# Performance work log

Hardware: AMD Instinct MI355X
Metric: run time of the kernel (lower is better)

## Reference

```python
import jax, jax.numpy as jnp
import numpy as np

B, S, H, A = 16, 2048, 1024, 1024


def setup_inputs() -> dict:
    key = jax.random.key(0)
    k1, k2, k3 = jax.random.split(key, 3)
    x = jax.random.normal(k1, (B, S, H), dtype=jnp.float32)
    # learned params (nn.Parameter tensors in the torch module)
    w_a = jax.random.normal(k2, (H, A), dtype=jnp.float32) * 0.02
    query = jax.random.normal(k3, (H, A), dtype=jnp.float32) * 0.02
    return {"x": x, "w_a": w_a, "query": query}


def reference(x, w_a, query):
    # semantic attention: values = x
    key = jnp.tanh(x @ w_a)          # [B, S, A]
    q = x @ query                    # [B, S, A]  (per-token semantic query)
    # temp[b, s, t] = q[b, s] . key[b, t]
    temp = jnp.einsum('bsa,bta->bst', q, key)  # [B, S, S]
    seq_len = x.shape[1]
    # softmax mask: strictly-upper triangle = -inf, lower+diag = 0 (causal)
    causal = jnp.triu(jnp.ones((seq_len, seq_len), dtype=bool), k=1)
    softmax_mask = jnp.where(causal, -jnp.inf, 0.0).astype(x.dtype)
    d = jax.nn.softmax(temp + softmax_mask, axis=-1)  # [B, S, S]
    a = d @ x                        # [B, S, H]
    return (a, d)
```

## Files before the change

### kernel.cpp

```cpp
#include <hip/hip_runtime.h>

typedef _Float16 f16x8 __attribute__((ext_vector_type(8)));
typedef float f32x4 __attribute__((ext_vector_type(4)));
typedef unsigned short u16;
typedef u16 u16x4 __attribute__((ext_vector_type(4)));
typedef u16 u16x8 __attribute__((ext_vector_type(8)));

#define NBATCH 16
#define NSEQ   2048
#define NHID   1024
#define MALL   (NBATCH * NSEQ)

__device__ __forceinline__ u16 f16_rne(float x) {
    _Float16 h = (_Float16)x;
    return __builtin_bit_cast(u16, h);
}
__device__ __forceinline__ float fast_tanh(float x) {
    float e = __expf(2.0f * x);
    return 1.0f - 2.0f / (e + 1.0f);
}

#define GLOAD16(g, l) __builtin_amdgcn_global_lds(0)
#undef GLOAD16
#define GLOAD16(g, l) __builtin_amdgcn_global_load_lds(                         \
    (const __attribute__((address_space(1))) unsigned int*)(g),                 \
    (__attribute__((address_space(3))) unsigned int*)(l), 16, 0, 0)


#define NOPS ((void)0)
#define VMW4 asm volatile("s_waitcnt vmcnt(4)" ::: "memory");
#define VMW0 asm volatile("s_waitcnt vmcnt(0)" ::: "memory");

#define MMPH(MH, NH)                                                           \
    MM(acc[MH][NH][0][0], 0, (NH)*2+0); MM(acc[MH][NH][0][1], 0, (NH)*2+1);    \
    MM(acc[MH][NH][1][0], 1, (NH)*2+0); MM(acc[MH][NH][1][1], 1, (NH)*2+1);    \
    MM(acc[MH][NH][2][0], 2, (NH)*2+0); MM(acc[MH][NH][2][1], 2, (NH)*2+1);    \
    MM(acc[MH][NH][3][0], 3, (NH)*2+0); MM(acc[MH][NH][3][1], 3, (NH)*2+1);    \
    MM(acc[MH][NH][0][0], 4, (NH)*2+4); MM(acc[MH][NH][0][1], 4, (NH)*2+5);    \
    MM(acc[MH][NH][1][0], 5, (NH)*2+4); MM(acc[MH][NH][1][1], 5, (NH)*2+5);    \
    MM(acc[MH][NH][2][0], 6, (NH)*2+4); MM(acc[MH][NH][2][1], 6, (NH)*2+5);    \
    MM(acc[MH][NH][3][0], 7, (NH)*2+4); MM(acc[MH][NH][3][1], 7, (NH)*2+5);

#define PH_SYNC                                                                \
    __builtin_amdgcn_s_barrier();                                              \
    asm volatile("s_waitcnt lgkmcnt(0)" ::: "memory");                         \
    __builtin_amdgcn_sched_barrier(0);

#define TILE8(C, S1, S2, S3, S4, W) {                                          \
                                                                \
    LDA(0,C,0,0); LDA(1,C,0,0); LDA(2,C,0,0); LDA(3,C,0,0);                    \
    LDA(4,C,0,1); LDA(5,C,0,1); LDA(6,C,0,1); LDA(7,C,0,1);                    \
    LDB(0,C,0,0); LDB(1,C,0,0); LDB(4,C,0,1); LDB(5,C,0,1);                    \
    S1;                                                                        \
    PH_SYNC                                                                    \
    __builtin_amdgcn_s_setprio(1); MMPH(0,0) __builtin_amdgcn_s_setprio(0);    \
    __builtin_amdgcn_s_barrier();                                              \
                                                                \
    LDB(2,C,1,0); LDB(3,C,1,0); LDB(6,C,1,1); LDB(7,C,1,1);                    \
    S2;                                                                        \
    PH_SYNC                                                                    \
    __builtin_amdgcn_s_setprio(1); MMPH(0,1) __builtin_amdgcn_s_setprio(0);    \
    __builtin_amdgcn_s_barrier();                                              \
                                                                \
    LDA(0,C,1,0); LDA(1,C,1,0); LDA(2,C,1,0); LDA(3,C,1,0);                    \
    LDA(4,C,1,1); LDA(5,C,1,1); LDA(6,C,1,1); LDA(7,C,1,1);                    \
    S3;                                                                        \
    PH_SYNC                                                                    \
    __builtin_amdgcn_s_setprio(1); MMPH(1,0) __builtin_amdgcn_s_setprio(0);    \
    __builtin_amdgcn_s_barrier();                                              \
                                                                \
    S4;                                                                        \
    PH_SYNC                                                                    \
    __builtin_amdgcn_s_setprio(1); MMPH(1,1) __builtin_amdgcn_s_setprio(0);    \
    W;                                                                         \
    __builtin_amdgcn_s_barrier();                                              \
}

__device__ __forceinline__ void gemm_core64(
    const u16* __restrict__ Ap, int Arow0,
    const u16* __restrict__ Bp, int Brow0,
    u16* lds, f32x4 (&acc)[2][2][4][2])
{
    int tid = threadIdx.x;
    int l = tid & 63, w = tid >> 6;
    int wr = w >> 2, wc = w & 3;
    int fr = l & 15, sg = l >> 4;

    f16x8 ah[8], bh[8];

    auto LDA = [&](int i, int C, int MH, int KH) {
        int rb = MH * 128 + wr * 64 + (i & 3) * 16 + fr;
        int sl = ((KH * 4 + sg) ^ (rb & 7)) * 8;
        ah[i] = *(const f16x8*)&lds[C * 32768 + rb * 64 + sl];
    };
    auto LDB = [&](int j, int C, int NH, int KH) {
        int rb = NH * 128 + wc * 32 + (j & 1) * 16 + fr;
        int sl = ((KH * 4 + sg) ^ (rb & 7)) * 8;
        bh[j] = *(const f16x8*)&lds[C * 32768 + 16384 + rb * 64 + sl];
    };
    auto MM = [&](f32x4& d, int i, int j) {
        d = __builtin_amdgcn_mfma_f32_16x16x32_f16(ah[i], bh[j], d, 0, 0, 0);
    };
    auto STA = [&](int C, int H, int T) {
        int rg = Arow0 + H * 128 + w * 8 + (l >> 3);
        const u16* s = Ap + (size_t)rg * 1024 + (size_t)T * 64
                       + ((l & 7) ^ (rg & 7)) * 8;
        u16* d = &lds[C * 32768 + (H * 128 + w * 8) * 64];
        GLOAD16(s, d);
        GLOAD16(s + (size_t)64 * 1024, d + 64 * 64);
    };
    auto STB = [&](int C, int H, int T) {
        int rg = Brow0 + H * 128 + w * 8 + (l >> 3);
        const u16* s = Bp + (size_t)rg * 1024 + (size_t)T * 64
                       + ((l & 7) ^ (rg & 7)) * 8;
        u16* d = &lds[C * 32768 + 16384 + (H * 128 + w * 8) * 64];
        GLOAD16(s, d);
        GLOAD16(s + (size_t)64 * 1024, d + 64 * 64);
    };

    STA(0, 0, 0); STA(0, 1, 0); STB(0, 0, 0); STB(0, 1, 0);
    STA(1, 0, 1); STB(1, 0, 1);
    VMW4
    __builtin_amdgcn_s_barrier();

    for (int u = 0; u < 13; u += 2) {
        TILE8(0, STA(1,1,u+1), STB(1,1,u+1), STA(0,0,u+2), STB(0,0,u+2), VMW4)
        TILE8(1, STA(0,1,u+2), STB(0,1,u+2), STA(1,0,u+3), STB(1,0,u+3), VMW4)
    }
    TILE8(0, STA(1,1,15), STB(1,1,15), NOPS, NOPS, VMW0)
    TILE8(1, NOPS, NOPS, NOPS, NOPS, NOPS)
}

__global__ __launch_bounds__(256) void wprep_kernel(
    const float* __restrict__ wa, const float* __restrict__ qu,
    u16* __restrict__ wT)
{
    int idx = blockIdx.x * 256 + threadIdx.x;
    int h = idx >> 10, n = idx & 1023;
    wT[(size_t)n * 1024 + h]          = f16_rne(wa[idx] * 64.0f);
    wT[(size_t)(1024 + n) * 1024 + h] = f16_rne(qu[idx] * 64.0f);
}

__global__ __launch_bounds__(256) void xprep_kernel(
    const float* __restrict__ x, u16* __restrict__ xT,
    u16* __restrict__ x_f16)
{
    __shared__ u16 tile[64][68];
    int b = blockIdx.z;
    int t0 = blockIdx.x * 64;
    int h0 = blockIdx.y * 64;
    const float* xb = x + ((size_t)b * NSEQ + t0) * NHID + h0;
    int tid = threadIdx.x;
    int tl = tid >> 4;
    int hl = (tid & 15) * 4;
    #pragma unroll
    for (int i = 0; i < 4; i++) {
        int r = i * 16 + tl;
        float4 v = *(const float4*)&xb[(size_t)r * NHID + hl];
        u16x4 hv;
        hv[0] = f16_rne(v.x); hv[1] = f16_rne(v.y);
        hv[2] = f16_rne(v.z); hv[3] = f16_rne(v.w);
        *(u16x4*)&tile[r][hl] = hv;
        *(u16x4*)&x_f16[((size_t)(b * NSEQ) + t0 + r) * NHID + h0 + hl] = hv;
    }
    __syncthreads();
    u16* xTb = xT + ((size_t)b * NHID + h0) * NSEQ + t0;
    int hl2 = tid >> 4;
    int tl2 = (tid & 15) * 4;
    #pragma unroll
    for (int i = 0; i < 4; i++) {
        int hh = i * 16 + hl2;
        u16x4 o;
        o[0] = tile[tl2 + 0][hh]; o[1] = tile[tl2 + 1][hh];
        o[2] = tile[tl2 + 2][hh]; o[3] = tile[tl2 + 3][hh];
        *(u16x4*)&xTb[(size_t)hh * NSEQ + tl2] = o;
    }
}

__global__ __launch_bounds__(512, 2) void k1_gemm(
    const u16* __restrict__ x_f16, const u16* __restrict__ wT,
    u16* __restrict__ k_f16, u16* __restrict__ q_f16)
{
    extern __shared__ u16 lds[];
    int wg = blockIdx.x;
    int nid = (wg & 7) * 128 + (wg >> 3);
    int n0 = (nid & 7) * 256;
    int m0 = (nid >> 3) * 256;
    bool is_key = (n0 < 1024);

    f32x4 acc[2][2][4][2] = {};
    gemm_core64(x_f16, m0, wT, n0, lds, acc);

    int tid = threadIdx.x;
    int l = tid & 63, w = tid >> 6;
    int wr = w >> 2, wc = w & 3;
    int fr = l & 15, fq = l >> 4;
    int nb = is_key ? n0 : (n0 - 1024);
    u16* outp = is_key ? k_f16 : q_f16;
    #pragma unroll
    for (int mh = 0; mh < 2; mh++)
    #pragma unroll
    for (int nh = 0; nh < 2; nh++)
    #pragma unroll
    for (int m = 0; m < 4; m++)
    #pragma unroll
    for (int n = 0; n < 2; n++)
    #pragma unroll
    for (int j = 0; j < 4; j++) {
        int grow = m0 + mh * 128 + wr * 64 + m * 16 + fq * 4 + j;
        int c    = nb + nh * 128 + wc * 32 + n * 16 + fr;
        float v = acc[mh][nh][m][n][j] * 0.015625f;
        outp[(size_t)grow * 1024 + c] = f16_rne(is_key ? fast_tanh(v) : v);
    }
}

__global__ __launch_bounds__(512, 2) void k2_logits(
    const u16* __restrict__ q_f16, const u16* __restrict__ k_f16,
    float* __restrict__ dmat)
{
    extern __shared__ u16 lds[];
    int wg = blockIdx.x;
    int nid = (wg & 7) * 72 + (wg >> 3);
    int b = nid / 36;
    int lin = nid - b * 36;
    int st = 0;
    while ((st + 1) * (st + 2) / 2 <= lin) st++;
    int tt = lin - st * (st + 1) / 2;
    int s0 = st * 256, t0 = tt * 256;
    int base = b * NSEQ;

    f32x4 acc[2][2][4][2] = {};
    gemm_core64(q_f16, base + s0, k_f16, base + t0, lds, acc);

    float* db = dmat + (size_t)b * NSEQ * NSEQ;
    int tid = threadIdx.x;
    int l = tid & 63, w = tid >> 6;
    int wr = w >> 2, wc = w & 3;
    int fr = l & 15, fq = l >> 4;
    #pragma unroll
    for (int mh = 0; mh < 2; mh++)
    #pragma unroll
    for (int nh = 0; nh < 2; nh++)
    #pragma unroll
    for (int m = 0; m < 4; m++)
    #pragma unroll
    for (int n = 0; n < 2; n++)
    #pragma unroll
    for (int j = 0; j < 4; j++) {
        int s = s0 + mh * 128 + wr * 64 + m * 16 + fq * 4 + j;
        int t = t0 + nh * 128 + wc * 32 + n * 16 + fr;
        if (t <= s) db[(size_t)s * NSEQ + t] = acc[mh][nh][m][n][j];
    }
}

__global__ __launch_bounds__(256) void k3_softmax(
    float* __restrict__ dmat, u16* __restrict__ d_f16)
{
    __shared__ float redm[4];
    __shared__ float reds[4];
    int rowid = blockIdx.x;
    int s = rowid & (NSEQ - 1);
    float* row = dmat + (size_t)rowid * NSEQ;
    int tid = threadIdx.x;
    int lane = tid & 63, w = tid >> 6;
    int t0 = tid * 8;

    float v[8];
    if (t0 <= s) {
        float4 a = *(const float4*)&row[t0];
        float4 c = *(const float4*)&row[t0 + 4];
        v[0] = a.x; v[1] = a.y; v[2] = a.z; v[3] = a.w;
        v[4] = c.x; v[5] = c.y; v[6] = c.z; v[7] = c.w;
        #pragma unroll
        for (int i = 0; i < 8; i++) if (t0 + i > s) v[i] = -INFINITY;
    } else {
        #pragma unroll
        for (int i = 0; i < 8; i++) v[i] = -INFINITY;
    }

    float m = -INFINITY;
    #pragma unroll
    for (int i = 0; i < 8; i++) m = fmaxf(m, v[i]);
    #pragma unroll
    for (int off = 32; off > 0; off >>= 1) m = fmaxf(m, __shfl_xor(m, off));
    if (lane == 0) redm[w] = m;
    __syncthreads();
    m = fmaxf(fmaxf(redm[0], redm[1]), fmaxf(redm[2], redm[3]));

    float sum = 0.f;
    float ev[8];
    #pragma unroll
    for (int i = 0; i < 8; i++) {
        ev[i] = (t0 + i <= s) ? __expf(v[i] - m) : 0.f;
        sum += ev[i];
    }
    #pragma unroll
    for (int off = 32; off > 0; off >>= 1) sum += __shfl_xor(sum, off);
    if (lane == 0) reds[w] = sum;
    __syncthreads();
    sum = reds[0] + reds[1] + reds[2] + reds[3];
    float inv = 1.0f / sum;

    float4 o0, o1;
    o0.x = ev[0] * inv; o0.y = ev[1] * inv; o0.z = ev[2] * inv; o0.w = ev[3] * inv;
    o1.x = ev[4] * inv; o1.y = ev[5] * inv; o1.z = ev[6] * inv; o1.w = ev[7] * inv;
    *(float4*)&row[t0] = o0;
    *(float4*)&row[t0 + 4] = o1;
    if (t0 <= ((s >> 7) << 7) + 127) {
        u16x8 bv;
        bv[0] = f16_rne(o0.x); bv[1] = f16_rne(o0.y); bv[2] = f16_rne(o0.z); bv[3] = f16_rne(o0.w);
        bv[4] = f16_rne(o1.x); bv[5] = f16_rne(o1.y); bv[6] = f16_rne(o1.z); bv[7] = f16_rne(o1.w);
        *(u16x8*)&d_f16[(size_t)rowid * NSEQ + t0] = bv;
    }
}

__global__ __launch_bounds__(256) void k4_av(
    const u16* __restrict__ d_f16,
    const u16* __restrict__ xT,
    float* __restrict__ aout)
{
    __shared__ u16 sa[128 * 32];
    __shared__ u16 sb[128 * 32];

    int wg = blockIdx.x;
    int nid = (wg & 7) * 256 + (wg >> 3);
    int n0 = (nid & 7) * 128;
    int s0 = ((nid >> 3) & 15) * 128;
    int b = nid >> 7;

    int tid = threadIdx.x;
    int lane = tid & 63;
    int w = tid >> 6;
    int wr = w >> 1, wc = w & 1;

    int srow = w * 16 + (lane >> 2);
    int sslot = ((lane & 3) ^ ((lane >> 3) & 3)) * 8;

    const u16* pa = d_f16 + (size_t)(b * NSEQ + s0 + srow) * NSEQ + sslot;
    const u16* pb = xT + ((size_t)b * NHID + n0 + srow) * NSEQ + sslot;
    u16* da0 = &sa[(w * 16) * 32];  u16* da1 = &sa[(64 + w * 16) * 32];
    u16* db0 = &sb[(w * 16) * 32];  u16* db1 = &sb[(64 + w * 16) * 32];
    const size_t R64 = (size_t)64 * NSEQ;

    int fr = lane & 15, sg = lane >> 4;
    int rsl = (sg ^ ((fr >> 1) & 3)) * 8;

    f32x4 acc[4][4] = {};
    int kmax = s0 + 128;

    for (int kk = 0; kk < kmax; kk += 32) {
        __syncthreads();
        GLOAD16(pa + kk, da0); GLOAD16(pa + kk + R64, da1);
        GLOAD16(pb + kk, db0); GLOAD16(pb + kk + R64, db1);
        __syncthreads();

        f16x8 af[4], bf[4];
        #pragma unroll
        for (int m = 0; m < 4; m++)
            af[m] = *(const f16x8*)&sa[(wr * 64 + m * 16 + fr) * 32 + rsl];
        #pragma unroll
        for (int n = 0; n < 4; n++)
            bf[n] = *(const f16x8*)&sb[(wc * 64 + n * 16 + fr) * 32 + rsl];
        #pragma unroll
        for (int m = 0; m < 4; m++)
            #pragma unroll
            for (int n = 0; n < 4; n++)
                acc[m][n] = __builtin_amdgcn_mfma_f32_16x16x32_f16(af[m], bf[n], acc[m][n], 0, 0, 0);
    }

    float* ab = aout + (size_t)b * NSEQ * NHID;
    int fq = lane >> 4;
    #pragma unroll
    for (int m = 0; m < 4; m++)
        #pragma unroll
        for (int n = 0; n < 4; n++)
            #pragma unroll
            for (int j = 0; j < 4; j++) {
                int s = s0 + wr * 64 + m * 16 + fq * 4 + j;
                int h = n0 + wc * 64 + n * 16 + fr;
                ab[(size_t)s * NHID + h] = acc[m][n][j];
            }
}

extern "C" void kernel_launch(void* const* d_in, const int* in_sizes, int n_in,
                              void* d_out, int out_size, void* d_ws, size_t ws_size,
                              hipStream_t stream)
{
    const float* x     = (const float*)d_in[0];
    const float* w_a   = (const float*)d_in[1];
    const float* query = (const float*)d_in[2];

    float* aout = (float*)d_out;
    float* dmat = aout + (size_t)NBATCH * NSEQ * NHID;

    char* p = (char*)d_ws;
    u16* q_f16  = (u16*)p; p += (size_t)MALL * 1024 * 2;
    u16* x_f16  = (u16*)p; p += (size_t)MALL * 1024 * 2;
    u16* k_f16  = (u16*)p; p += (size_t)MALL * 1024 * 2;
    u16* d_f16  = x_f16;
    u16* xT     = (u16*)p; p += (size_t)MALL * 1024 * 2;
    u16* wT     = (u16*)p; p += (size_t)2048 * 1024 * 2;
    (void)ws_size; (void)in_sizes; (void)n_in; (void)out_size;

    hipFuncSetAttribute((const void*)k1_gemm,
                        hipFuncAttributeMaxDynamicSharedMemorySize, 131072);
    hipFuncSetAttribute((const void*)k2_logits,
                        hipFuncAttributeMaxDynamicSharedMemorySize, 131072);

    wprep_kernel<<<dim3(4096), 256, 0, stream>>>(w_a, query, wT);
    xprep_kernel<<<dim3(32, 16, 16), 256, 0, stream>>>(x, xT, x_f16);
    k1_gemm<<<dim3(1024), 512, 131072, stream>>>(x_f16, wT, k_f16, q_f16);
    k2_logits<<<dim3(576), 512, 131072, stream>>>(q_f16, k_f16, dmat);
    k3_softmax<<<dim3(32768), 256, 0, stream>>>(dmat, d_f16);
    k4_av<<<dim3(2048), 256, 0, stream>>>(d_f16, xT, aout);
}
```

Before: 550.3 us.

## Reuse pipelined 256x256 GEMM core for AV product and move upper-triangle zeroing into logits kernel

```diff
diff --git a/kernel.cpp b/kernel.cpp
--- a/kernel.cpp
+++ b/kernel.cpp
@@ -20,8 +20,6 @@
     return 1.0f - 2.0f / (e + 1.0f);
 }
 
-#define GLOAD16(g, l) __builtin_amdgcn_global_lds(0)
-#undef GLOAD16
 #define GLOAD16(g, l) __builtin_amdgcn_global_load_lds(                         \
     (const __attribute__((address_space(1))) unsigned int*)(g),                 \
     (__attribute__((address_space(3))) unsigned int*)(l), 16, 0, 0)
@@ -76,10 +74,11 @@
     __builtin_amdgcn_s_barrier();                                              \
 }
 
+template<int AST, int BST>
 __device__ __forceinline__ void gemm_core64(
     const u16* __restrict__ Ap, int Arow0,
     const u16* __restrict__ Bp, int Brow0,
-    u16* lds, f32x4 (&acc)[2][2][4][2])
+    int nt, u16* lds, f32x4 (&acc)[2][2][4][2])
 {
     int tid = threadIdx.x;
     int l = tid & 63, w = tid >> 6;
@@ -103,19 +102,19 @@
     };
     auto STA = [&](int C, int H, int T) {
         int rg = Arow0 + H * 128 + w * 8 + (l >> 3);
-        const u16* s = Ap + (size_t)rg * 1024 + (size_t)T * 64
+        const u16* s = Ap + (size_t)rg * AST + (size_t)T * 64
                        + ((l & 7) ^ (rg & 7)) * 8;
         u16* d = &lds[C * 32768 + (H * 128 + w * 8) * 64];
         GLOAD16(s, d);
-        GLOAD16(s + (size_t)64 * 1024, d + 64 * 64);
+        GLOAD16(s + (size_t)64 * AST, d + 64 * 64);
     };
     auto STB = [&](int C, int H, int T) {
         int rg = Brow0 + H * 128 + w * 8 + (l >> 3);
-        const u16* s = Bp + (size_t)rg * 1024 + (size_t)T * 64
+        const u16* s = Bp + (size_t)rg * BST + (size_t)T * 64
                        + ((l & 7) ^ (rg & 7)) * 8;
         u16* d = &lds[C * 32768 + 16384 + (H * 128 + w * 8) * 64];
         GLOAD16(s, d);
-        GLOAD16(s + (size_t)64 * 1024, d + 64 * 64);
+        GLOAD16(s + (size_t)64 * BST, d + 64 * 64);
     };
 
     STA(0, 0, 0); STA(0, 1, 0); STB(0, 0, 0); STB(0, 1, 0);
@@ -123,11 +122,11 @@
     VMW4
     __builtin_amdgcn_s_barrier();
 
-    for (int u = 0; u < 13; u += 2) {
+    for (int u = 0; u + 2 < nt; u += 2) {
         TILE8(0, STA(1,1,u+1), STB(1,1,u+1), STA(0,0,u+2), STB(0,0,u+2), VMW4)
         TILE8(1, STA(0,1,u+2), STB(0,1,u+2), STA(1,0,u+3), STB(1,0,u+3), VMW4)
     }
-    TILE8(0, STA(1,1,15), STB(1,1,15), NOPS, NOPS, VMW0)
+    TILE8(0, STA(1,1,nt-1), STB(1,1,nt-1), NOPS, NOPS, VMW0)
     TILE8(1, NOPS, NOPS, NOPS, NOPS, NOPS)
 }
 
@@ -189,7 +188,7 @@
     bool is_key = (n0 < 1024);
 
     f32x4 acc[2][2][4][2] = {};
-    gemm_core64(x_f16, m0, wT, n0, lds, acc);
+    gemm_core64<1024, 1024>(x_f16, m0, wT, n0, 16, lds, acc);
 
     int tid = threadIdx.x;
     int l = tid & 63, w = tid >> 6;
@@ -220,6 +219,27 @@
 {
     extern __shared__ u16 lds[];
     int wg = blockIdx.x;
+    int tid = threadIdx.x;
+
+    if (wg >= 576) {
+        int z = wg - 576;
+        int b = z / 28;
+        int lin = z - b * 28;
+        int tt = 1;
+        while ((tt + 1) * tt / 2 <= lin) tt++;
+        int st = lin - tt * (tt - 1) / 2;
+        float* db = dmat + (size_t)b * NSEQ * NSEQ;
+        size_t base = (size_t)(st * 256) * NSEQ + tt * 256;
+        float4 zz = make_float4(0.f, 0.f, 0.f, 0.f);
+        #pragma unroll
+        for (int i = 0; i < 32; i++) {
+            int e = i * 512 + tid;
+            int row = e >> 6, c4 = e & 63;
+            *(float4*)&db[base + (size_t)row * NSEQ + c4 * 4] = zz;
+        }
+        return;
+    }
+
     int nid = (wg & 7) * 72 + (wg >> 3);
     int b = nid / 36;
     int lin = nid - b * 36;
@@ -230,10 +250,9 @@
     int base = b * NSEQ;
 
     f32x4 acc[2][2][4][2] = {};
-    gemm_core64(q_f16, base + s0, k_f16, base + t0, lds, acc);
+    gemm_core64<1024, 1024>(q_f16, base + s0, k_f16, base + t0, 16, lds, acc);
 
     float* db = dmat + (size_t)b * NSEQ * NSEQ;
-    int tid = threadIdx.x;
     int l = tid & 63, w = tid >> 6;
     int wr = w >> 2, wc = w & 3;
     int fr = l & 15, fq = l >> 4;
@@ -249,7 +268,7 @@
     for (int j = 0; j < 4; j++) {
         int s = s0 + mh * 128 + wr * 64 + m * 16 + fq * 4 + j;
         int t = t0 + nh * 128 + wc * 32 + n * 16 + fr;
-        if (t <= s) db[(size_t)s * NSEQ + t] = acc[mh][nh][m][n][j];
+        db[(size_t)s * NSEQ + t] = (t <= s) ? acc[mh][nh][m][n][j] : 0.0f;
     }
 }
 
@@ -304,9 +323,11 @@
     float4 o0, o1;
     o0.x = ev[0] * inv; o0.y = ev[1] * inv; o0.z = ev[2] * inv; o0.w = ev[3] * inv;
     o1.x = ev[4] * inv; o1.y = ev[5] * inv; o1.z = ev[6] * inv; o1.w = ev[7] * inv;
-    *(float4*)&row[t0] = o0;
-    *(float4*)&row[t0 + 4] = o1;
-    if (t0 <= ((s >> 7) << 7) + 127) {
+    if (t0 <= s) {
+        *(float4*)&row[t0] = o0;
+        *(float4*)&row[t0 + 4] = o1;
+    }
+    if (t0 < (((s >> 8) + 1) << 8)) {
         u16x8 bv;
         bv[0] = f16_rne(o0.x); bv[1] = f16_rne(o0.y); bv[2] = f16_rne(o0.z); bv[3] = f16_rne(o0.w);
         bv[4] = f16_rne(o1.x); bv[5] = f16_rne(o1.y); bv[6] = f16_rne(o1.z); bv[7] = f16_rne(o1.w);
@@ -314,72 +335,43 @@
     }
 }
 
-__global__ __launch_bounds__(256) void k4_av(
+__global__ __launch_bounds__(512, 2) void k4_av(
     const u16* __restrict__ d_f16,
     const u16* __restrict__ xT,
     float* __restrict__ aout)
 {
-    __shared__ u16 sa[128 * 32];
-    __shared__ u16 sb[128 * 32];
-
+    extern __shared__ u16 lds[];
     int wg = blockIdx.x;
-    int nid = (wg & 7) * 256 + (wg >> 3);
-    int n0 = (nid & 7) * 128;
-    int s0 = ((nid >> 3) & 15) * 128;
-    int b = nid >> 7;
-
-    int tid = threadIdx.x;
-    int lane = tid & 63;
-    int w = tid >> 6;
-    int wr = w >> 1, wc = w & 1;
-
-    int srow = w * 16 + (lane >> 2);
-    int sslot = ((lane & 3) ^ ((lane >> 3) & 3)) * 8;
-
-    const u16* pa = d_f16 + (size_t)(b * NSEQ + s0 + srow) * NSEQ + sslot;
-    const u16* pb = xT + ((size_t)b * NHID + n0 + srow) * NSEQ + sslot;
-    u16* da0 = &sa[(w * 16) * 32];  u16* da1 = &sa[(64 + w * 16) * 32];
-    u16* db0 = &sb[(w * 16) * 32];  u16* db1 = &sb[(64 + w * 16) * 32];
-    const size_t R64 = (size_t)64 * NSEQ;
-
-    int fr = lane & 15, sg = lane >> 4;
-    int rsl = (sg ^ ((fr >> 1) & 3)) * 8;
-
-    f32x4 acc[4][4] = {};
-    int kmax = s0 + 128;
-
-    for (int kk = 0; kk < kmax; kk += 32) {
-        __syncthreads();
-        GLOAD16(pa + kk, da0); GLOAD16(pa + kk + R64, da1);
-        GLOAD16(pb + kk, db0); GLOAD16(pb + kk + R64, db1);
-        __syncthreads();
-
-        f16x8 af[4], bf[4];
-        #pragma unroll
-        for (int m = 0; m < 4; m++)
-            af[m] = *(const f16x8*)&sa[(wr * 64 + m * 16 + fr) * 32 + rsl];
-        #pragma unroll
-        for (int n = 0; n < 4; n++)
-            bf[n] = *(const f16x8*)&sb[(wc * 64 + n * 16 + fr) * 32 + rsl];
-        #pragma unroll
-        for (int m = 0; m < 4; m++)
-            #pragma unroll
-            for (int n = 0; n < 4; n++)
-                acc[m][n] = __builtin_amdgcn_mfma_f32_16x16x32_f16(af[m], bf[n], acc[m][n], 0, 0, 0);
-    }
+    int st = 7 - (wg >> 6);
+    int rem = wg & 63;
+    int b = rem >> 2;
+    int ntile = rem & 3;
+    int s0 = st * 256;
+    int n0 = ntile * 256;
+    int nt = 4 * (st + 1);
+
+    f32x4 acc[2][2][4][2] = {};
+    gemm_core64<2048, 2048>(d_f16, b * 2048 + s0, xT, b * 1024 + n0, nt, lds, acc);
 
     float* ab = aout + (size_t)b * NSEQ * NHID;
-    int fq = lane >> 4;
+    int tid = threadIdx.x;
+    int l = tid & 63, w = tid >> 6;
+    int wr = w >> 2, wc = w & 3;
+    int fr = l & 15, fq = l >> 4;
+    #pragma unroll
+    for (int mh = 0; mh < 2; mh++)
+    #pragma unroll
+    for (int nh = 0; nh < 2; nh++)
     #pragma unroll
     for (int m = 0; m < 4; m++)
-        #pragma unroll
-        for (int n = 0; n < 4; n++)
-            #pragma unroll
-            for (int j = 0; j < 4; j++) {
-                int s = s0 + wr * 64 + m * 16 + fq * 4 + j;
-                int h = n0 + wc * 64 + n * 16 + fr;
-                ab[(size_t)s * NHID + h] = acc[m][n][j];
-            }
+    #pragma unroll
+    for (int n = 0; n < 2; n++)
+    #pragma unroll
+    for (int j = 0; j < 4; j++) {
+        int s = s0 + mh * 128 + wr * 64 + m * 16 + fq * 4 + j;
+        int c = n0 + nh * 128 + wc * 32 + n * 16 + fr;
+        ab[(size_t)s * NHID + c] = acc[mh][nh][m][n][j];
+    }
 }
 
 extern "C" void kernel_launch(void* const* d_in, const int* in_sizes, int n_in,
@@ -406,11 +398,13 @@
                         hipFuncAttributeMaxDynamicSharedMemorySize, 131072);
     hipFuncSetAttribute((const void*)k2_logits,
                         hipFuncAttributeMaxDynamicSharedMemorySize, 131072);
+    hipFuncSetAttribute((const void*)k4_av,
+                        hipFuncAttributeMaxDynamicSharedMemorySize, 131072);
 
     wprep_kernel<<<dim3(4096), 256, 0, stream>>>(w_a, query, wT);
     xprep_kernel<<<dim3(32, 16, 16), 256, 0, stream>>>(x, xT, x_f16);
     k1_gemm<<<dim3(1024), 512, 131072, stream>>>(x_f16, wT, k_f16, q_f16);
-    k2_logits<<<dim3(576), 512, 131072, stream>>>(q_f16, k_f16, dmat);
+    k2_logits<<<dim3(1024), 512, 131072, stream>>>(q_f16, k_f16, dmat);
     k3_softmax<<<dim3(32768), 256, 0, stream>>>(dmat, d_f16);
-    k4_av<<<dim3(2048), 256, 0, stream>>>(d_f16, xT, aout);
-}
+    k4_av<<<dim3(512), 512, 131072, stream>>>(d_f16, xT, aout);
+}
```

After: 502.7 us, median of 2. 1.09x faster.
